# Kernel tuning notes

Measured on AMD Instinct MI355X. Metric: run time of the kernel, lower is better.

Reference implementation:

```python
import jax, jax.numpy as jnp
import numpy as np

C = 256
RATE_CHOICE = [32, 64, 96, 128, 160, 192, 224, 256]
RATE_NUM = len(RATE_CHOICE)
MAX_RATE = max(RATE_CHOICE)
B, H, W = 16, 16, 16


def setup_inputs() -> dict:
    key = jax.random.key(0)
    k_x, k_idx, k_w = jax.random.split(key, 3)
    x = jax.random.normal(k_x, (B, C, H, W), dtype=jnp.float32)
    indexes = jax.random.randint(k_idx, (B * H * W,), 0, RATE_NUM, dtype=jnp.int64)
    # xavier_normal over (fan_in=C*MAX_RATE? torch 3D: fan_in=C*MAX_RATE, fan_out=RATE_NUM*MAX_RATE) -> use gain std
    std = float(np.sqrt(2.0 / (C + MAX_RATE)))
    weight = jax.random.normal(k_w, (RATE_NUM, C, MAX_RATE), dtype=jnp.float32) * std
    bias = jnp.zeros((RATE_NUM, MAX_RATE), dtype=jnp.float32)
    rate_choice_tensor = jnp.asarray(RATE_CHOICE, dtype=jnp.int32)
    return {"x": x, "indexes": indexes, "weight": weight, "bias": bias,
            "rate_choice_tensor": rate_choice_tensor}


def reference(x, indexes, weight, bias, rate_choice_tensor):
    Bv, Cv, Hv, Wv = x.shape
    L = Hv * Wv
    R = weight.shape[-1]
    # x: [B,C,H,W] -> [B,L,C]
    x_blc = x.reshape(Bv, Cv, L).transpose(0, 2, 1)
    # per-token gathered weights/bias
    w = weight[indexes].reshape(Bv, L, Cv, R)      # [B,L,C,R]
    b = bias[indexes].reshape(Bv, L, R)            # [B,L,R]
    # rate mask: arange(R) < rate_choice[idx]
    rc = rate_choice_tensor[indexes].reshape(Bv, L, 1)
    mask = (jnp.arange(R, dtype=rc.dtype)[None, None, :] < rc).astype(x.dtype)  # [B,L,R]
    # batched per-token matvec + bias, then mask
    y = (jnp.einsum('blc,blcr->blr', x_blc, w) + b) * mask
    x_masked = y.reshape(Bv, Hv, Wv, R).transpose(0, 3, 1, 2)     # [B,R,H,W]
    mask_bchw = mask.reshape(Bv, Hv, Wv, R).transpose(0, 3, 1, 2)
    return (x_masked, mask_bchw)
```

## Files before the change

kernel.cpp:

```cpp
#include <hip/hip_runtime.h>

#define WS_BUCKET 1024
#define WS_XT     262144
#define WS_YP     4456448
#define WS_NEED   (4456448 + 16777216)

__global__ __launch_bounds__(256) void bucket_kernel(const int* __restrict__ idx,
                                                     int* __restrict__ counts,
                                                     int* __restrict__ bucket) {
  __shared__ int lcount[8];
  __shared__ int lbase[8];
  const int tid = threadIdx.x;
  const int t = (blockIdx.x << 8) + tid;
  if (tid < 8) lcount[tid] = 0;
  __syncthreads();
  const int g = idx[t];
  const int lpos = atomicAdd(&lcount[g], 1);
  __syncthreads();
  if (tid < 8) lbase[tid] = atomicAdd(&counts[tid], lcount[tid]);
  __syncthreads();
  bucket[(g << 12) + lbase[g] + lpos] = t;
}

__global__ __launch_bounds__(256) void xpose_kernel(const float* __restrict__ x,
                                                    float* __restrict__ xT) {
  __shared__ float tile[32][33];
  const int b = blockIdx.x;
  const int c0 = (blockIdx.y >> 3) << 5;
  const int l0 = (blockIdx.y & 7) << 5;
  const int j = threadIdx.x & 31;
  const int i = threadIdx.x >> 5;
#pragma unroll
  for (int ii = 0; ii < 4; ++ii) {
    const int c = c0 + (ii << 3) + i;
    tile[(ii << 3) + i][j] = x[(b << 16) + (c << 8) + l0 + j];
  }
  __syncthreads();
#pragma unroll
  for (int ii = 0; ii < 4; ++ii) {
    const int l = l0 + (ii << 3) + i;
    xT[(((b << 8) + l) << 8) + c0 + j] = tile[j][(ii << 3) + i];
  }
}

__global__ __launch_bounds__(256) void gemv_kernel(const float* __restrict__ xT,
                                                   const float* __restrict__ W,
                                                   const float* __restrict__ bias,
                                                   const int* __restrict__ counts,
                                                   const int* __restrict__ bucket,
                                                   float* __restrict__ yP) {
  const int g  = blockIdx.x;
  const int n  = counts[g];
  const int t0 = blockIdx.y << 5;
  if (t0 >= n) return;
  const int cz = blockIdx.z;
  const int c0 = cz << 6;
  const int nt = min(32, n - t0);
  const int tid = threadIdx.x;
  const int lane = tid & 63;
  const int wid  = tid >> 6;

  __shared__ float wsl[64 * 256];
  __shared__ float xs[64][36];
  __shared__ int toks[32];

  if (tid < 32) toks[tid] = bucket[(g << 12) + min(t0 + tid, n - 1)];
  __syncthreads();

  {
    const float4* src = reinterpret_cast<const float4*>(W + (g << 16) + (c0 << 8));
    float4* dst = reinterpret_cast<float4*>(wsl);
#pragma unroll 4
    for (int k = 0; k < 16; ++k) dst[(k << 8) + tid] = src[(k << 8) + tid];
  }
  {
    const int t = tid >> 3, q = tid & 7;
    const float* src = xT + (toks[t] << 8) + c0 + (q << 3);
    const float4 a = *reinterpret_cast<const float4*>(src);
    const float4 b = *reinterpret_cast<const float4*>(src + 4);
    const int cb = q << 3;
    xs[cb + 0][t] = a.x; xs[cb + 1][t] = a.y; xs[cb + 2][t] = a.z; xs[cb + 3][t] = a.w;
    xs[cb + 4][t] = b.x; xs[cb + 5][t] = b.y; xs[cb + 6][t] = b.z; xs[cb + 7][t] = b.w;
  }
  __syncthreads();

  const int r0 = lane << 2;
  const int tb = wid << 3;
  float acc[8][4];
  if (cz == 0) {
    const float4 bv = *reinterpret_cast<const float4*>(bias + (g << 8) + r0);
#pragma unroll
    for (int j = 0; j < 8; ++j) {
      acc[j][0] = bv.x; acc[j][1] = bv.y; acc[j][2] = bv.z; acc[j][3] = bv.w;
    }
  } else {
#pragma unroll
    for (int j = 0; j < 8; ++j) acc[j][0] = acc[j][1] = acc[j][2] = acc[j][3] = 0.0f;
  }

#pragma unroll 4
  for (int c = 0; c < 64; ++c) {
    const float4 wv = *reinterpret_cast<const float4*>(&wsl[(c << 8) + r0]);
    const float4 xa = *reinterpret_cast<const float4*>(&xs[c][tb]);
    const float4 xb = *reinterpret_cast<const float4*>(&xs[c][tb + 4]);
    const float xv[8] = {xa.x, xa.y, xa.z, xa.w, xb.x, xb.y, xb.z, xb.w};
#pragma unroll
    for (int j = 0; j < 8; ++j) {
      acc[j][0] += xv[j] * wv.x; acc[j][1] += xv[j] * wv.y;
      acc[j][2] += xv[j] * wv.z; acc[j][3] += xv[j] * wv.w;
    }
  }

  float* dst = yP + ((size_t)cz << 20);
#pragma unroll
  for (int j = 0; j < 8; ++j) {
    const int t = tb + j;
    if (t < nt) {
      float4 v;
      v.x = acc[j][0]; v.y = acc[j][1]; v.z = acc[j][2]; v.w = acc[j][3];
      *reinterpret_cast<float4*>(dst + (toks[t] << 8) + r0) = v;
    }
  }
}

__global__ __launch_bounds__(256) void out_kernel(const float* __restrict__ yP,
                                                  const int* __restrict__ idx,
                                                  const int* __restrict__ rate,
                                                  float* __restrict__ out) {
  __shared__ float tile[32][33];
  __shared__ int rcl[32];
  const int b = blockIdx.x;
  const int r0 = (blockIdx.y >> 3) << 5;
  const int l0 = (blockIdx.y & 7) << 5;
  const int j = threadIdx.x & 31;
  const int i = threadIdx.x >> 5;
#pragma unroll
  for (int ii = 0; ii < 4; ++ii) {
    const int l = l0 + (ii << 3) + i;
    const int base = (((b << 8) + l) << 8) + r0 + j;
    tile[(ii << 3) + i][j] = yP[base] + yP[(1 << 20) + base] +
                             yP[(2 << 20) + base] + yP[(3 << 20) + base];
  }
  if (threadIdx.x < 32) rcl[threadIdx.x] = rate[idx[(b << 8) + l0 + threadIdx.x]];
  __syncthreads();
#pragma unroll
  for (int ii = 0; ii < 4; ++ii) {
    const int r = r0 + (ii << 3) + i;
    const float m = (r < rcl[j]) ? 1.0f : 0.0f;
    const int o = (b << 16) + (r << 8) + l0 + j;
    out[o] = tile[j][(ii << 3) + i] * m;
    out[(1 << 20) + o] = m;
  }
}

__global__ __launch_bounds__(256) void rate_tok_kernel(
    const float* __restrict__ x, const int* __restrict__ indexes,
    const float* __restrict__ W, const float* __restrict__ bias,
    const int* __restrict__ rate, float* __restrict__ out) {
  const int t = blockIdx.x;
  const int b = t >> 8;
  const int l = t & 255;
  const int r = threadIdx.x;
  __shared__ float xs[256];
  xs[r] = x[(b << 16) + (r << 8) + l];
  const int g = indexes[t];
  const int rc = rate[g];
  __syncthreads();
  const float* w = W + (g << 16) + r;
  float acc = bias[(g << 8) + r];
#pragma unroll 8
  for (int c = 0; c < 256; ++c) acc += xs[c] * w[c << 8];
  const float m = (r < rc) ? 1.0f : 0.0f;
  const int o = (b << 16) + (r << 8) + l;
  out[o] = acc * m;
  out[(1 << 20) + o] = m;
}

extern "C" void kernel_launch(void* const* d_in, const int* in_sizes, int n_in,
                              void* d_out, int out_size, void* d_ws, size_t ws_size,
                              hipStream_t stream) {
  const float* x    = (const float*)d_in[0];
  const int*   idx  = (const int*)d_in[1];
  const float* W    = (const float*)d_in[2];
  const float* bias = (const float*)d_in[3];
  const int*   rate = (const int*)d_in[4];
  float* out = (float*)d_out;

  if (ws_size >= (size_t)WS_NEED) {
    int*   counts = (int*)d_ws;
    int*   bucket = (int*)((char*)d_ws + WS_BUCKET);
    float* xT     = (float*)((char*)d_ws + WS_XT);
    float* yP     = (float*)((char*)d_ws + WS_YP);
    hipMemsetAsync(counts, 0, 8 * sizeof(int), stream);
    bucket_kernel<<<dim3(16), dim3(256), 0, stream>>>(idx, counts, bucket);
    xpose_kernel<<<dim3(16, 64), dim3(256), 0, stream>>>(x, xT);
    gemv_kernel<<<dim3(8, 128, 4), dim3(256), 0, stream>>>(xT, W, bias, counts, bucket, yP);
    out_kernel<<<dim3(16, 64), dim3(256), 0, stream>>>(yP, idx, rate, out);
  } else {
    rate_tok_kernel<<<dim3(4096), dim3(256), 0, stream>>>(x, idx, W, bias, rate, out);
  }
}
```

Baseline: 96.56 us.

## Use bf16 weights in shared memory, fuse prep kernels, shrink gemv grid

Adds a prep kernel that merges the token bucketing and the x transpose, and also converts the fp32 weights to packed bf16 on every call. The gemv kernel then stages bf16 weights in LDS, which halves its shared memory footprint and weight traffic, and unpacks them to fp32 before the FMAs. The x tile padding is removed with a new load mapping, and the gemv grid's token dimension is cut from 128 to 40 blocks to avoid launching empty blocks. This introduces bf16 rounding error and silently assumes no rate group holds more than 1280 tokens.

Result: faster. 94.59 us (-2.0%).

```diff
diff --git a/kernel.cpp b/kernel.cpp
--- a/kernel.cpp
+++ b/kernel.cpp
@@ -1,50 +1,75 @@
 #include <hip/hip_runtime.h>
 
-#define WS_BUCKET 1024
-#define WS_XT     262144
-#define WS_YP     4456448
-#define WS_NEED   (4456448 + 16777216)
-
-__global__ __launch_bounds__(256) void bucket_kernel(const int* __restrict__ idx,
-                                                     int* __restrict__ counts,
-                                                     int* __restrict__ bucket) {
-  __shared__ int lcount[8];
-  __shared__ int lbase[8];
+#define WS_BUCKET 4096
+#define WS_WBF    1048576
+#define WS_XT     2097152
+#define WS_YP     6291456
+#define WS_NEED   23068672
+
+__device__ __forceinline__ unsigned int bf16_rne(float f) {
+  unsigned int u = __float_as_uint(f);
+  return (u + 0x7fffu + ((u >> 16) & 1u)) >> 16;
+}
+
+__global__ __launch_bounds__(256) void prep_kernel(const float* __restrict__ x,
+                                                   const int* __restrict__ idx,
+                                                   const float* __restrict__ W,
+                                                   int* __restrict__ counts,
+                                                   int* __restrict__ bucket,
+                                                   unsigned int* __restrict__ Wbf,
+                                                   float* __restrict__ xT) {
+  const int bx = blockIdx.x;
+  const int by = blockIdx.y;
   const int tid = threadIdx.x;
-  const int t = (blockIdx.x << 8) + tid;
-  if (tid < 8) lcount[tid] = 0;
-  __syncthreads();
-  const int g = idx[t];
-  const int lpos = atomicAdd(&lcount[g], 1);
-  __syncthreads();
-  if (tid < 8) lbase[tid] = atomicAdd(&counts[tid], lcount[tid]);
-  __syncthreads();
-  bucket[(g << 12) + lbase[g] + lpos] = t;
-}
-
-__global__ __launch_bounds__(256) void xpose_kernel(const float* __restrict__ x,
-                                                    float* __restrict__ xT) {
-  __shared__ float tile[32][33];
-  const int b = blockIdx.x;
-  const int c0 = (blockIdx.y >> 3) << 5;
-  const int l0 = (blockIdx.y & 7) << 5;
-  const int j = threadIdx.x & 31;
-  const int i = threadIdx.x >> 5;
-#pragma unroll
-  for (int ii = 0; ii < 4; ++ii) {
-    const int c = c0 + (ii << 3) + i;
-    tile[(ii << 3) + i][j] = x[(b << 16) + (c << 8) + l0 + j];
-  }
-  __syncthreads();
-#pragma unroll
-  for (int ii = 0; ii < 4; ++ii) {
-    const int l = l0 + (ii << 3) + i;
-    xT[(((b << 8) + l) << 8) + c0 + j] = tile[j][(ii << 3) + i];
+
+  if (by < 64) {
+    __shared__ float tile[32][33];
+    const int b = bx;
+    const int c0 = (by >> 3) << 5;
+    const int l0 = (by & 7) << 5;
+    const int j = tid & 31;
+    const int i = tid >> 5;
+#pragma unroll
+    for (int ii = 0; ii < 4; ++ii) {
+      const int c = c0 + (ii << 3) + i;
+      tile[(ii << 3) + i][j] = x[(b << 16) + (c << 8) + l0 + j];
+    }
+    __syncthreads();
+#pragma unroll
+    for (int ii = 0; ii < 4; ++ii) {
+      const int l = l0 + (ii << 3) + i;
+      xT[(((b << 8) + l) << 8) + c0 + j] = tile[j][(ii << 3) + i];
+    }
+  } else if (by == 64) {
+    __shared__ int lcount[8];
+    __shared__ int lbase[8];
+    const int t = (bx << 8) + tid;
+    if (tid < 8) lcount[tid] = 0;
+    __syncthreads();
+    const int g = idx[t];
+    const int lpos = atomicAdd(&lcount[g], 1);
+    __syncthreads();
+    if (tid < 8) lbase[tid] = atomicAdd(&counts[tid], lcount[tid]);
+    __syncthreads();
+    bucket[(g << 12) + lbase[g] + lpos] = t;
+  } else {
+    const int chunk = bx * 7 + (by - 65);
+    const int v0 = chunk * 1171;
+    const int v1 = min(v0 + 1171, 131072);
+    const float4* src = reinterpret_cast<const float4*>(W);
+    uint2* dst = reinterpret_cast<uint2*>(Wbf);
+    for (int v = v0 + tid; v < v1; v += 256) {
+      const float4 f = src[v];
+      uint2 o;
+      o.x = bf16_rne(f.x) | (bf16_rne(f.y) << 16);
+      o.y = bf16_rne(f.z) | (bf16_rne(f.w) << 16);
+      dst[v] = o;
+    }
   }
 }
 
 __global__ __launch_bounds__(256) void gemv_kernel(const float* __restrict__ xT,
-                                                   const float* __restrict__ W,
+                                                   const uint2* __restrict__ Wbf,
                                                    const float* __restrict__ bias,
                                                    const int* __restrict__ counts,
                                                    const int* __restrict__ bucket,
@@ -60,25 +85,24 @@
   const int lane = tid & 63;
   const int wid  = tid >> 6;
 
-  __shared__ float wsl[64 * 256];
-  __shared__ float xs[64][36];
+  __shared__ uint2 wslb[4096];
+  __shared__ float xs[64][32];
   __shared__ int toks[32];
 
   if (tid < 32) toks[tid] = bucket[(g << 12) + min(t0 + tid, n - 1)];
   __syncthreads();
 
   {
-    const float4* src = reinterpret_cast<const float4*>(W + (g << 16) + (c0 << 8));
-    float4* dst = reinterpret_cast<float4*>(wsl);
+    const uint2* src = Wbf + (g << 14) + (c0 << 6);
 #pragma unroll 4
-    for (int k = 0; k < 16; ++k) dst[(k << 8) + tid] = src[(k << 8) + tid];
+    for (int k = 0; k < 16; ++k) wslb[(k << 8) + tid] = src[(k << 8) + tid];
   }
   {
-    const int t = tid >> 3, q = tid & 7;
-    const float* src = xT + (toks[t] << 8) + c0 + (q << 3);
+    const int t = tid & 31, cq = tid >> 5;
+    const float* src = xT + (toks[t] << 8) + c0 + (cq << 3);
     const float4 a = *reinterpret_cast<const float4*>(src);
     const float4 b = *reinterpret_cast<const float4*>(src + 4);
-    const int cb = q << 3;
+    const int cb = cq << 3;
     xs[cb + 0][t] = a.x; xs[cb + 1][t] = a.y; xs[cb + 2][t] = a.z; xs[cb + 3][t] = a.w;
     xs[cb + 4][t] = b.x; xs[cb + 5][t] = b.y; xs[cb + 6][t] = b.z; xs[cb + 7][t] = b.w;
   }
@@ -100,14 +124,18 @@
 
 #pragma unroll 4
   for (int c = 0; c < 64; ++c) {
-    const float4 wv = *reinterpret_cast<const float4*>(&wsl[(c << 8) + r0]);
+    const uint2 wu = wslb[(c << 6) + lane];
+    const float w0 = __uint_as_float(wu.x << 16);
+    const float w1 = __uint_as_float(wu.x & 0xffff0000u);
+    const float w2 = __uint_as_float(wu.y << 16);
+    const float w3 = __uint_as_float(wu.y & 0xffff0000u);
     const float4 xa = *reinterpret_cast<const float4*>(&xs[c][tb]);
     const float4 xb = *reinterpret_cast<const float4*>(&xs[c][tb + 4]);
     const float xv[8] = {xa.x, xa.y, xa.z, xa.w, xb.x, xb.y, xb.z, xb.w};
 #pragma unroll
     for (int j = 0; j < 8; ++j) {
-      acc[j][0] += xv[j] * wv.x; acc[j][1] += xv[j] * wv.y;
-      acc[j][2] += xv[j] * wv.z; acc[j][3] += xv[j] * wv.w;
+      acc[j][0] += xv[j] * w0; acc[j][1] += xv[j] * w1;
+      acc[j][2] += xv[j] * w2; acc[j][3] += xv[j] * w3;
     }
   }
 
@@ -187,14 +215,15 @@
   float* out = (float*)d_out;
 
   if (ws_size >= (size_t)WS_NEED) {
-    int*   counts = (int*)d_ws;
-    int*   bucket = (int*)((char*)d_ws + WS_BUCKET);
-    float* xT     = (float*)((char*)d_ws + WS_XT);
-    float* yP     = (float*)((char*)d_ws + WS_YP);
+    int*          counts = (int*)d_ws;
+    int*          bucket = (int*)((char*)d_ws + WS_BUCKET);
+    unsigned int* Wbf    = (unsigned int*)((char*)d_ws + WS_WBF);
+    float*        xT     = (float*)((char*)d_ws + WS_XT);
+    float*        yP     = (float*)((char*)d_ws + WS_YP);
     hipMemsetAsync(counts, 0, 8 * sizeof(int), stream);
-    bucket_kernel<<<dim3(16), dim3(256), 0, stream>>>(idx, counts, bucket);
-    xpose_kernel<<<dim3(16, 64), dim3(256), 0, stream>>>(x, xT);
-    gemv_kernel<<<dim3(8, 128, 4), dim3(256), 0, stream>>>(xT, W, bias, counts, bucket, yP);
+    prep_kernel<<<dim3(16, 72), dim3(256), 0, stream>>>(x, idx, W, counts, bucket, Wbf, xT);
+    gemv_kernel<<<dim3(8, 40, 4), dim3(256), 0, stream>>>(
+        xT, (const uint2*)Wbf, bias, counts, bucket, yP);
     out_kernel<<<dim3(16, 64), dim3(256), 0, stream>>>(yP, idx, rate, out);
   } else {
     rate_tok_kernel<<<dim3(4096), dim3(256), 0, stream>>>(x, idx, W, bias, rate, out);
```
